# Optimization experiments

Hardware: AMD Instinct MI355X
Metric: run time of the kernel (lower is better)

The kernel has to match this reference:

```python
import jax, jax.numpy as jnp
import numpy as np

B, S, D = 4, 2048, 1024
H = 16
DH = D // H


def setup_inputs() -> dict:
    key = jax.random.key(0)
    ks = jax.random.split(key, 9)
    s = 0.02
    return {
        "x": jax.random.normal(ks[0], (B, S, D), dtype=jnp.float32),
        "Wq": jax.random.normal(ks[1], (D, D), dtype=jnp.float32) * s,
        "bq": jax.random.normal(ks[2], (D,), dtype=jnp.float32) * s,
        "Wk": jax.random.normal(ks[3], (D, D), dtype=jnp.float32) * s,
        "bk": jax.random.normal(ks[4], (D,), dtype=jnp.float32) * s,
        "Wv": jax.random.normal(ks[5], (D, D), dtype=jnp.float32) * s,
        "bv": jax.random.normal(ks[6], (D,), dtype=jnp.float32) * s,
        "Wo": jax.random.normal(ks[7], (D, D), dtype=jnp.float32) * s,
        "bo": jax.random.normal(ks[8], (D,), dtype=jnp.float32) * s,
    }


def _split_heads(t):
    # [B,S,D] -> [B,H,S,DH]
    b, s, d = t.shape
    return t.reshape(b, s, H, DH).transpose(0, 2, 1, 3)


def reference(x, Wq, bq, Wk, bk, Wv, bv, Wo, bo):
    q = _split_heads(x @ Wq.T + bq)
    k = _split_heads(x @ Wk.T + bk)
    v = _split_heads(x @ Wv.T + bv)
    scale = 1.0 / np.sqrt(DH).astype(np.float32)
    scores = jnp.einsum("bhqd,bhkd->bhqk", q, k) * scale  # [B,H,S,S]
    s = scores.shape[-2]
    causal = jnp.tril(jnp.ones((s, s), dtype=bool))
    scores = jnp.where(causal[None, None], scores, -jnp.inf)
    probs = jax.nn.softmax(scores, axis=-1)
    out = jnp.einsum("bhqk,bhkd->bhqd", probs, v)  # [B,H,S,DH]
    out = out.transpose(0, 2, 1, 3).reshape(x.shape[0], s, D)
    return out @ Wo.T + bo
```

## Files before the change

### kernel.cpp

```cpp
#include <hip/hip_runtime.h>
#include <hip/hip_bf16.h>
#include <cstdint>
#include <cstddef>


typedef unsigned short u16;
typedef __bf16 bf16x8 __attribute__((ext_vector_type(8)));
typedef float  f32x4  __attribute__((ext_vector_type(4)));

__device__ __forceinline__ u16 f2bf(float f) {
  unsigned u = __float_as_uint(f);
  unsigned r = u + 0x7fffu + ((u >> 16) & 1u);
  return (u16)(r >> 16);
}

__device__ __forceinline__ void llds16(const u16* g, u16* l) {
  __builtin_amdgcn_global_load_lds(
      (const __attribute__((address_space(1))) void*)g,
      (__attribute__((address_space(3))) void*)l, 16, 0, 0);
}

__global__ void cast_bf16_kernel(const float* __restrict__ in, u16* __restrict__ out, int n4) {
  int i = blockIdx.x * blockDim.x + threadIdx.x;
  if (i >= n4) return;
  float4 f = ((const float4*)in)[i];
  ushort4 u;
  u.x = f2bf(f.x); u.y = f2bf(f.y); u.z = f2bf(f.z); u.w = f2bf(f.w);
  ((ushort4*)out)[i] = u;
}

__global__ void cast4_kernel(const float* __restrict__ a, const float* __restrict__ b,
                             const float* __restrict__ c, const float* __restrict__ d,
                             u16* __restrict__ oa, u16* __restrict__ ob,
                             u16* __restrict__ oc, u16* __restrict__ od, int n4) {
  const int w = blockIdx.y;
  const float* src = (w == 0) ? a : (w == 1) ? b : (w == 2) ? c : d;
  u16* dst = (w == 0) ? oa : (w == 1) ? ob : (w == 2) ? oc : od;
  int i = blockIdx.x * blockDim.x + threadIdx.x;
  if (i >= n4) return;
  float4 f = ((const float4*)src)[i];
  ushort4 u;
  u.x = f2bf(f.x); u.y = f2bf(f.y); u.z = f2bf(f.z); u.w = f2bf(f.w);
  ((ushort4*)dst)[i] = u;
}

__global__ __launch_bounds__(512) void gemm_qkv_256(
    const u16* __restrict__ A, const u16* __restrict__ Bw,
    const float* __restrict__ b0, const float* __restrict__ b1, const float* __restrict__ b2,
    u16* __restrict__ qkv_out)
{
  __shared__ u16 lds[57344];

  const int tid = threadIdx.x;
  const int lane = tid & 63;
  const int wave = tid >> 6;

  const int bid = (int)blockIdx.x;
  const int xcd = bid & 7;
  const int idx = bid >> 3;
  const int mt = (xcd << 2) | (idx & 3);
  const int nt = idx >> 2;
  const int m0 = mt << 8;
  const int n0 = nt * 192;

  const int warp_m = wave >> 2;
  const int warp_n = wave & 3;
  const int wm = warp_m << 7;
  const int wn = warp_n * 48;
  const int fr = lane & 15;
  const int g  = lane >> 4;

  const int srow = tid >> 3;
  const int schk = ((tid & 7) ^ (srow & 7)) << 3;
  const u16* pA = A  + (size_t)(m0 + srow) * 1024 + schk;
  const u16* pB = Bw + (size_t)(n0 + srow) * 1024 + schk;

  const int rsw0 = ((g    ) ^ (fr & 7)) << 3;
  const int rsw1 = ((g ^ 4) ^ (fr & 7)) << 3;

  const u16* Ab0 = lds + (size_t)(wm + fr) * 64;
  const u16* Bb0 = lds + 16384 + (size_t)(wn + fr) * 64;
  const u16* Ab1 = Ab0 + 28672;
  const u16* Bb1 = Bb0 + 28672;

  f32x4 acc[8][3];
  const f32x4 zero = {0.f, 0.f, 0.f, 0.f};
#pragma unroll
  for (int i = 0; i < 8; i++)
#pragma unroll
    for (int j = 0; j < 3; j++) acc[i][j] = zero;

  bf16x8 a_[8][2];
  bf16x8 b_[3][2];

  auto stageA = [&](int kt, int buf, int half) {
    const u16* src = pA + (size_t)half * 131072 + (kt << 6);
    u16* dst = lds + buf * 28672 + half * 8192 + tid * 8;
    llds16(src, dst);
    llds16(src + 65536, dst + 4096);
  };
  auto stageB0 = [&](int kt, int buf) {
    const u16* src = pB + (kt << 6);
    u16* dst = lds + buf * 28672 + 16384 + tid * 8;
    llds16(src, dst);
    llds16(src + 65536, dst + 4096);
  };
  auto stageB1 = [&](int kt, int buf) {
    const u16* src = pB + 131072 + (kt << 6);
    u16* dst = lds + buf * 28672 + 24576 + tid * 8;
    llds16(src, dst);
  };
  auto loadA4 = [&](const u16* Ab, int ib) {
#pragma unroll
    for (int ii = 0; ii < 4; ii++) {
      const u16* r = Ab + (ib + ii) * 1024;
      a_[ib + ii][0] = *(const bf16x8*)(r + rsw0);
      a_[ib + ii][1] = *(const bf16x8*)(r + rsw1);
    }
  };
  auto loadB = [&](const u16* Bb, int j0, int nj) {
#pragma unroll
    for (int jj = 0; jj < 3; jj++) {
      if (jj < nj) {
        const u16* r = Bb + (j0 + jj) * 1024;
        b_[j0 + jj][0] = *(const bf16x8*)(r + rsw0);
        b_[j0 + jj][1] = *(const bf16x8*)(r + rsw1);
      }
    }
  };
  auto mfmaJ01 = [&](int ib) {
    __builtin_amdgcn_s_setprio(1);
#pragma unroll
    for (int jj = 0; jj < 2; jj++)
#pragma unroll
      for (int ii = 0; ii < 4; ii++) {
        acc[ib+ii][jj] = __builtin_amdgcn_mfma_f32_16x16x32_bf16(
            a_[ib+ii][0], b_[jj][0], acc[ib+ii][jj], 0, 0, 0);
        acc[ib+ii][jj] = __builtin_amdgcn_mfma_f32_16x16x32_bf16(
            a_[ib+ii][1], b_[jj][1], acc[ib+ii][jj], 0, 0, 0);
      }
    __builtin_amdgcn_s_setprio(0);
  };
  auto mfmaJ2 = [&]() {
    __builtin_amdgcn_s_setprio(1);
#pragma unroll
    for (int ii = 0; ii < 8; ii++) {
      acc[ii][2] = __builtin_amdgcn_mfma_f32_16x16x32_bf16(
          a_[ii][0], b_[2][0], acc[ii][2], 0, 0, 0);
      acc[ii][2] = __builtin_amdgcn_mfma_f32_16x16x32_bf16(
          a_[ii][1], b_[2][1], acc[ii][2], 0, 0, 0);
    }
    __builtin_amdgcn_s_setprio(0);
  };

  stageA(0, 0, 0);
  stageA(0, 0, 1);
  stageB0(0, 0);
  stageB1(0, 0);
  stageA(1, 1, 0);
  asm volatile("s_waitcnt vmcnt(2)" ::: "memory");
  __builtin_amdgcn_s_barrier();

  const int NTI = 8;
  for (int t = 0; t < NTI; ++t) {
    const bool st = (t < NTI - 1);
    const int ka = 2 * t + 1;
    const int kb = 2 * t + 2;
    const int kc = 2 * t + 3;

    loadA4(Ab0, 0); loadB(Bb0, 0, 2);
    stageA(ka, 1, 1);
    __builtin_amdgcn_s_barrier();
    mfmaJ01(0);
    __builtin_amdgcn_s_barrier();
    loadA4(Ab0, 4);
    stageB0(ka, 1);
    __builtin_amdgcn_s_barrier();
    mfmaJ01(4);
    __builtin_amdgcn_s_barrier();
    loadB(Bb0, 2, 1);
    stageB1(ka, 1);
    if (st) stageA(kb, 0, 0);
    __builtin_amdgcn_s_barrier();
    mfmaJ2();
    if (st) { asm volatile("s_waitcnt vmcnt(2)" ::: "memory"); }
    else    { asm volatile("s_waitcnt vmcnt(0)" ::: "memory"); }
    __builtin_amdgcn_s_barrier();

    loadA4(Ab1, 0); loadB(Bb1, 0, 2);
    if (st) stageA(kb, 0, 1);
    __builtin_amdgcn_s_barrier();
    mfmaJ01(0);
    __builtin_amdgcn_s_barrier();
    loadA4(Ab1, 4);
    if (st) stageB0(kb, 0);
    __builtin_amdgcn_s_barrier();
    mfmaJ01(4);
    __builtin_amdgcn_s_barrier();
    loadB(Bb1, 2, 1);
    if (st) { stageB1(kb, 0); stageA(kc, 1, 0); }
    __builtin_amdgcn_s_barrier();
    mfmaJ2();
    if (st) { asm volatile("s_waitcnt vmcnt(2)" ::: "memory"); }
    __builtin_amdgcn_s_barrier();
  }

  __syncthreads();
  const int bI  = m0 >> 11;
  const int s0m = m0 & 2047;
#pragma unroll
  for (int j = 0; j < 3; j++) {
    const int ncol = n0 + wn + j * 16 + fr;
    const int which = ncol >> 10;
    const float bb = ((which == 0) ? b0 : (which == 1) ? b1 : b2)[ncol & 1023];
    const float post = (which == 0) ? 0.18033688011f : 1.0f;
    const int cl = wn + j * 16 + fr;
#pragma unroll
    for (int i = 0; i < 8; i++) {
#pragma unroll
      for (int r = 0; r < 4; r++) {
        const int row = wm + i * 16 + g * 4 + r;
        lds[row * 200 + cl] = f2bf((acc[i][j][r] + bb) * post);
      }
    }
  }
  __syncthreads();
  const int part = tid & 7;
#pragma unroll
  for (int p = 0; p < 12; p++) {
    const int hc = p >> 2;
    const int ml = ((p & 3) << 6) + (tid >> 3);
    const int ncol0 = n0 + hc * 64;
    const int which = ncol0 >> 10;
    const int h = (ncol0 >> 6) & 15;
    const bf16x8 v = *(const bf16x8*)(lds + ml * 200 + hc * 64 + part * 8);
    *(bf16x8*)(qkv_out + (size_t)which * 8388608 +
               ((size_t)(bI * 16 + h) * 2048 + s0m + ml) * 64 + part * 8) = v;
  }
}

__global__ __launch_bounds__(512) void gemm_o_256(
    const u16* __restrict__ A, const u16* __restrict__ Bw,
    const float* __restrict__ bo, float* __restrict__ out)
{
  __shared__ u16 lds[49152];

  const int tid = threadIdx.x;
  const int lane = tid & 63;
  const int wave = tid >> 6;

  const int bid = (int)blockIdx.x;
  const int xcd = bid & 7;
  const int idx = bid >> 3;
  const int mt = (xcd << 2) | (idx & 3);
  const int nt = idx >> 2;
  const int m0 = mt << 8;
  const int n0 = nt << 7;

  const int warp_m = wave >> 2;
  const int warp_n = wave & 3;
  const int wm = warp_m << 7;
  const int wn = warp_n << 5;
  const int fr = lane & 15;
  const int g  = lane >> 4;

  const int srow = tid >> 3;
  const int schk = ((tid & 7) ^ (srow & 7)) << 3;
  const u16* pA = A  + (size_t)(m0 + srow) * 1024 + schk;
  const u16* pB = Bw + (size_t)(n0 + srow) * 1024 + schk;

  const int rsw0 = ((g    ) ^ (fr & 7)) << 3;
  const int rsw1 = ((g ^ 4) ^ (fr & 7)) << 3;

  const u16* Ab0 = lds + (size_t)(wm + fr) * 64;
  const u16* Bb0 = lds + 16384 + (size_t)(wn + fr) * 64;
  const u16* Ab1 = Ab0 + 24576;
  const u16* Bb1 = Bb0 + 24576;

  f32x4 acc[8][2];
  const f32x4 zero = {0.f, 0.f, 0.f, 0.f};
#pragma unroll
  for (int i = 0; i < 8; i++)
#pragma unroll
    for (int j = 0; j < 2; j++) acc[i][j] = zero;

  bf16x8 a_[8][2];
  bf16x8 b_[2][2];

  auto stageA = [&](int kt, int buf, int half) {
    const u16* src = pA + (size_t)half * 131072 + (kt << 6);
    u16* dst = lds + buf * 24576 + half * 8192 + tid * 8;
    llds16(src, dst);
    llds16(src + 65536, dst + 4096);
  };
  auto stageB = [&](int kt, int buf) {
    const u16* src = pB + (kt << 6);
    u16* dst = lds + buf * 24576 + 16384 + tid * 8;
    llds16(src, dst);
    llds16(src + 65536, dst + 4096);
  };
  auto loadA4 = [&](const u16* Ab, int ib) {
#pragma unroll
    for (int ii = 0; ii < 4; ii++) {
      const u16* r = Ab + (ib + ii) * 1024;
      a_[ib + ii][0] = *(const bf16x8*)(r + rsw0);
      a_[ib + ii][1] = *(const bf16x8*)(r + rsw1);
    }
  };
  auto loadB2 = [&](const u16* Bb) {
#pragma unroll
    for (int jj = 0; jj < 2; jj++) {
      const u16* r = Bb + jj * 1024;
      b_[jj][0] = *(const bf16x8*)(r + rsw0);
      b_[jj][1] = *(const bf16x8*)(r + rsw1);
    }
  };
  auto mfma16 = [&](int ib) {
    __builtin_amdgcn_s_setprio(1);
#pragma unroll
    for (int jj = 0; jj < 2; jj++)
#pragma unroll
      for (int ii = 0; ii < 4; ii++) {
        acc[ib+ii][jj] = __builtin_amdgcn_mfma_f32_16x16x32_bf16(
            a_[ib+ii][0], b_[jj][0], acc[ib+ii][jj], 0, 0, 0);
        acc[ib+ii][jj] = __builtin_amdgcn_mfma_f32_16x16x32_bf16(
            a_[ib+ii][1], b_[jj][1], acc[ib+ii][jj], 0, 0, 0);
      }
    __builtin_amdgcn_s_setprio(0);
  };
  auto mfma8 = [&](int ib, int jj) {
    __builtin_amdgcn_s_setprio(1);
#pragma unroll
    for (int ii = 0; ii < 4; ii++) {
      acc[ib+ii][jj] = __builtin_amdgcn_mfma_f32_16x16x32_bf16(
          a_[ib+ii][0], b_[jj][0], acc[ib+ii][jj], 0, 0, 0);
      acc[ib+ii][jj] = __builtin_amdgcn_mfma_f32_16x16x32_bf16(
          a_[ib+ii][1], b_[jj][1], acc[ib+ii][jj], 0, 0, 0);
    }
    __builtin_amdgcn_s_setprio(0);
  };

  stageA(0, 0, 0);
  stageA(0, 0, 1);
  stageB(0, 0);
  stageA(1, 1, 0);
  asm volatile("s_waitcnt vmcnt(2)" ::: "memory");
  __builtin_amdgcn_s_barrier();

  const int NTI = 8;
  for (int t = 0; t < NTI; ++t) {
    const bool st = (t < NTI - 1);
    const int ka = 2 * t + 1;
    const int kb = 2 * t + 2;
    const int kc = 2 * t + 3;

    loadA4(Ab0, 0); loadB2(Bb0);
    stageA(ka, 1, 1);
    __builtin_amdgcn_s_barrier();
    mfma16(0);
    __builtin_amdgcn_s_barrier();
    loadA4(Ab0, 4);
    stageB(ka, 1);
    __builtin_amdgcn_s_barrier();
    mfma8(4, 0);
    __builtin_amdgcn_s_barrier();
    if (st) stageA(kb, 0, 0);
    __builtin_amdgcn_s_barrier();
    mfma8(4, 1);
    if (st) { asm volatile("s_waitcnt vmcnt(2)" ::: "memory"); }
    else    { asm volatile("s_waitcnt vmcnt(0)" ::: "memory"); }
    __builtin_amdgcn_s_barrier();

    loadA4(Ab1, 0); loadB2(Bb1);
    if (st) stageA(kb, 0, 1);
    __builtin_amdgcn_s_barrier();
    mfma16(0);
    __builtin_amdgcn_s_barrier();
    loadA4(Ab1, 4);
    if (st) stageB(kb, 0);
    __builtin_amdgcn_s_barrier();
    mfma8(4, 0);
    __builtin_amdgcn_s_barrier();
    if (st) stageA(kc, 1, 0);
    __builtin_amdgcn_s_barrier();
    mfma8(4, 1);
    if (st) { asm volatile("s_waitcnt vmcnt(2)" ::: "memory"); }
    __builtin_amdgcn_s_barrier();
  }

#pragma unroll
  for (int j = 0; j < 2; j++) {
    const int n = n0 + wn + j * 16 + fr;
    const float bb = bo[n];
#pragma unroll
    for (int i = 0; i < 8; i++) {
#pragma unroll
      for (int r = 0; r < 4; r++) {
        const int m = m0 + wm + i * 16 + g * 4 + r;
        out[(size_t)m * 1024 + n] = acc[i][j][r] + bb;
      }
    }
  }
}

__global__ __launch_bounds__(256) void transpose_v(const u16* __restrict__ V, u16* __restrict__ VT) {
  __shared__ u16 t_s[64 * 72];
  const int tid = threadIdx.x;
  const int st = blockIdx.x << 6;
  const int bh = blockIdx.y;
  const u16* src = V + ((size_t)bh * 2048 + st) * 64;
#pragma unroll
  for (int p = 0; p < 2; p++) {
    int i = p * 256 + tid;
    int row = i >> 3, ch = i & 7;
    bf16x8 v = *(const bf16x8*)(src + row * 64 + ch * 8);
    *(bf16x8*)(t_s + row * 72 + ch * 8) = v;
  }
  __syncthreads();
  u16* dst = VT + (size_t)bh * 131072 + st;
#pragma unroll
  for (int p = 0; p < 2; p++) {
    int i = p * 256 + tid;
    int dh = i >> 3, ch = i & 7;
    union { u16 s[8]; bf16x8 v; } u;
#pragma unroll
    for (int e = 0; e < 8; e++) u.s[e] = t_s[(ch * 8 + e) * 72 + dh];
    *(bf16x8*)(dst + (size_t)dh * 2048 + ch * 8) = u.v;
  }
}

__global__ __launch_bounds__(256, 3) void attn_fa(
    const u16* __restrict__ Qb, const u16* __restrict__ Kb,
    const u16* __restrict__ VT, u16* __restrict__ Ob)
{
  __shared__ u16 k_s[2 * 4096];
  __shared__ u16 v_s[2 * 4096];
  __shared__ u16 p_s[128 * 72];
  __shared__ float l_s[128];

  const int tid = threadIdx.x;
  const int lane = tid & 63;
  const int wave = tid >> 6;
  const int bid = (int)blockIdx.x;
  const int qt = 15 - (bid >> 6);
  const int bh = (((bid >> 3) & 7) << 3) | (bid & 7);
  const size_t head = (size_t)bh << 17;
  const int fr = lane & 15;
  const int g = lane >> 4;
  const int k8 = g << 3;
  const int q0 = qt << 7;
  const int wrow = wave << 5;

  bf16x8 aq[2][2];
#pragma unroll
  for (int f = 0; f < 2; f++) {
    const u16* qp = Qb + head + (size_t)(q0 + wrow + (f << 4) + fr) * 64;
    aq[f][0] = *(const bf16x8*)(qp + k8);
    aq[f][1] = *(const bf16x8*)(qp + 32 + k8);
  }

  const int r0 = tid >> 3, c0 = tid & 7;
  const int r1 = 32 + r0;
  const int koff0 = r0 * 64 + (((c0 ^ r0) & 7) << 3);
  const int koff1 = r1 * 64 + (((c0 ^ r1) & 7) << 3);
  const int voff0 = r0 * 2048 + (((c0 ^ r0) & 7) << 3);
  const int voff1 = r1 * 2048 + (((c0 ^ r1) & 7) << 3);
  int kaddr[4][2], vaddr[2][4];
#pragma unroll
  for (int j = 0; j < 4; j++) {
    const int kn = (j << 4) + fr;
    kaddr[j][0] = kn * 64 + (((g ^ kn) & 7) << 3);
    kaddr[j][1] = kn * 64 + ((((g + 4) ^ kn) & 7) << 3);
#pragma unroll
    for (int s2 = 0; s2 < 2; s2++)
      vaddr[s2][j] = kn * 64 + ((((s2 << 2) + g) ^ (kn & 7)) << 3);
  }
  u16* const prow0 = p_s + (wrow + fr) * 72;
  u16* const prow1 = p_s + (wrow + 16 + fr) * 72;
  const u16* Kbase = Kb + head;
  const u16* Vbase = VT + head;

  auto issueK = [&](int jt2, int buf) {
    const u16* Kt = Kbase + ((size_t)jt2 << 12);
    llds16(Kt + koff0, k_s + (buf << 12) + tid * 8);
    llds16(Kt + koff1, k_s + (buf << 12) + 2048 + tid * 8);
  };
  auto issueV = [&](int jt2, int buf) {
    const u16* Vt = Vbase + (jt2 << 6);
    llds16(Vt + voff0, v_s + (buf << 12) + tid * 8);
    llds16(Vt + voff1, v_s + (buf << 12) + 2048 + tid * 8);
  };

  f32x4 o_acc[2][4];
  const f32x4 zero = {0.f, 0.f, 0.f, 0.f};
#pragma unroll
  for (int f = 0; f < 2; f++)
#pragma unroll
    for (int j = 0; j < 4; j++) o_acc[f][j] = zero;
  float l_run[2] = {0.f, 0.f};

  const int jmax = 2 * qt + 1;
  const int jt_diag = 2 * qt + (wave >> 1);

  auto do_pv = [&](const u16* vs) {
#pragma unroll
    for (int s2 = 0; s2 < 2; s2++) {
      const bf16x8 ap0 = *(const bf16x8*)(prow0 + (s2 << 5) + k8);
      const bf16x8 ap1 = *(const bf16x8*)(prow1 + (s2 << 5) + k8);
#pragma unroll
      for (int j = 0; j < 4; j++) {
        const bf16x8 bv = *(const bf16x8*)(vs + vaddr[s2][j]);
        o_acc[0][j] = __builtin_amdgcn_mfma_f32_16x16x32_bf16(ap0, bv, o_acc[0][j], 0, 0, 0);
        o_acc[1][j] = __builtin_amdgcn_mfma_f32_16x16x32_bf16(ap1, bv, o_acc[1][j], 0, 0, 0);
      }
    }
  };

  auto do_s = [&](const u16* ks, bool dodiag, int jt) {
    f32x4 s_acc[2][4];
#pragma unroll
    for (int f = 0; f < 2; f++)
#pragma unroll
      for (int j = 0; j < 4; j++) s_acc[f][j] = zero;
#pragma unroll
    for (int j = 0; j < 4; j++) {
      const bf16x8 ka0 = *(const bf16x8*)(ks + kaddr[j][0]);
      const bf16x8 ka1 = *(const bf16x8*)(ks + kaddr[j][1]);
      s_acc[0][j] = __builtin_amdgcn_mfma_f32_16x16x32_bf16(ka0, aq[0][0], s_acc[0][j], 0, 0, 0);
      s_acc[0][j] = __builtin_amdgcn_mfma_f32_16x16x32_bf16(ka1, aq[0][1], s_acc[0][j], 0, 0, 0);
      s_acc[1][j] = __builtin_amdgcn_mfma_f32_16x16x32_bf16(ka0, aq[1][0], s_acc[1][j], 0, 0, 0);
      s_acc[1][j] = __builtin_amdgcn_mfma_f32_16x16x32_bf16(ka1, aq[1][1], s_acc[1][j], 0, 0, 0);
    }
#pragma unroll
    for (int f = 0; f < 2; f++) {
      const int qa = q0 + wrow + (f << 4) + fr;
      u16* prow = (f == 0) ? prow0 : prow1;
      if (dodiag) {
#pragma unroll
        for (int j = 0; j < 4; j++) {
          const int kb = (jt << 6) + (j << 4) + (g << 2);
          float p0 = (kb + 0 > qa) ? 0.f : __builtin_amdgcn_exp2f(s_acc[f][j][0]);
          float p1 = (kb + 1 > qa) ? 0.f : __builtin_amdgcn_exp2f(s_acc[f][j][1]);
          float p2 = (kb + 2 > qa) ? 0.f : __builtin_amdgcn_exp2f(s_acc[f][j][2]);
          float p3 = (kb + 3 > qa) ? 0.f : __builtin_amdgcn_exp2f(s_acc[f][j][3]);
          l_run[f] += (p0 + p1) + (p2 + p3);
          union { __hip_bfloat162 h; unsigned u; } ca, cb;
          ca.h = __float22bfloat162_rn(make_float2(p0, p1));
          cb.h = __float22bfloat162_rn(make_float2(p2, p3));
          *(uint2*)(prow + (j << 4) + (g << 2)) = make_uint2(ca.u, cb.u);
        }
      } else {
#pragma unroll
        for (int j = 0; j < 4; j++) {
          float p0 = __builtin_amdgcn_exp2f(s_acc[f][j][0]);
          float p1 = __builtin_amdgcn_exp2f(s_acc[f][j][1]);
          float p2 = __builtin_amdgcn_exp2f(s_acc[f][j][2]);
          float p3 = __builtin_amdgcn_exp2f(s_acc[f][j][3]);
          l_run[f] += (p0 + p1) + (p2 + p3);
          union { __hip_bfloat162 h; unsigned u; } ca, cb;
          ca.h = __float22bfloat162_rn(make_float2(p0, p1));
          cb.h = __float22bfloat162_rn(make_float2(p2, p3));
          *(uint2*)(prow + (j << 4) + (g << 2)) = make_uint2(ca.u, cb.u);
        }
      }
    }
  };

  issueK(0, 0);

  for (int jt = 0; jt <= jmax; jt++) {
    const int kb = jt & 1;
    __syncthreads();
    if (jt < jmax) issueK(jt + 1, kb ^ 1);
    issueV(jt, kb);
    if (jt > 0 && jt - 1 <= jt_diag) do_pv(v_s + ((kb ^ 1) << 12));
    if (jt <= jt_diag) do_s(k_s + (kb << 12), jt == jt_diag, jt);
  }
  __syncthreads();
  if (jt_diag == jmax) do_pv(v_s + ((jmax & 1) << 12));

#pragma unroll
  for (int f = 0; f < 2; f++) {
    float l = l_run[f];
    l += __shfl_xor(l, 16);
    l += __shfl_xor(l, 32);
    if (g == 0) l_s[wrow + (f << 4) + fr] = l;
  }
  const int b = bh >> 4, h = bh & 15;
#pragma unroll
  for (int f = 0; f < 2; f++) {
#pragma unroll
    for (int r = 0; r < 4; r++) {
      const int qloc = wrow + (f << 4) + (g << 2) + r;
      const float inv = 1.f / l_s[qloc];
      const int q_abs = q0 + qloc;
#pragma unroll
      for (int j = 0; j < 4; j++)
        Ob[((size_t)b * 2048 + q_abs) * 1024 + (h << 6) + (j << 4) + fr] =
            f2bf(o_acc[f][j][r] * inv);
    }
  }
}

extern "C" void kernel_launch(void* const* d_in, const int* in_sizes, int n_in,
                              void* d_out, int out_size, void* d_ws, size_t ws_size,
                              hipStream_t stream) {
  const float* x  = (const float*)d_in[0];
  const float* Wq = (const float*)d_in[1];
  const float* bq = (const float*)d_in[2];
  const float* Wk = (const float*)d_in[3];
  const float* bk = (const float*)d_in[4];
  const float* Wv = (const float*)d_in[5];
  const float* bv = (const float*)d_in[6];
  const float* Wo = (const float*)d_in[7];
  const float* bo = (const float*)d_in[8];
  float* out = (float*)d_out;

  char* ws = (char*)d_ws;
  u16* xb    = (u16*)(ws);
  u16* vT    = (u16*)(ws);
  u16* wqkv  = (u16*)(ws + 16777216);
  u16* wo    = (u16*)(ws + 23068672);
  u16* qkv   = (u16*)(ws + 25165824);
  u16* attnb = (u16*)(ws + 75497472);

  cast_bf16_kernel<<<8192, 256, 0, stream>>>(x, xb, 2097152);
  cast4_kernel<<<dim3(1024, 4), 256, 0, stream>>>(
      Wq, Wk, Wv, Wo, wqkv, wqkv + 1048576, wqkv + 2097152, wo, 262144);

  gemm_qkv_256<<<dim3(512), 512, 0, stream>>>(xb, wqkv, bq, bk, bv, qkv);

  transpose_v<<<dim3(32, 64), 256, 0, stream>>>(qkv + 16777216, vT);

  attn_fa<<<dim3(1024), 256, 0, stream>>>(qkv, qkv + 8388608, vT, attnb);

  gemm_o_256<<<dim3(256), 512, 0, stream>>>(attnb, wo, bo, out);
}
```

Baseline: 242.0 us.

## Merge cast kernels and reorder QKV GEMM into quadrant MFMA phases

Replaces the separate activation and weight cast kernels with a single launch covering x and all four weights, removing one kernel launch. The QKV GEMM inner loop is restructured into quadrant phases (4 A-rows by 1-2 B-columns) so only four A fragments are live at once, reducing register pressure at the cost of extra barriers and a different load/stage interleaving. The attention output buffer is aliased onto the V region of qkv, which assumes V is no longer needed once transposed into vT.

```diff
diff --git a/kernel.cpp b/kernel.cpp
--- a/kernel.cpp
+++ b/kernel.cpp
@@ -20,28 +20,30 @@
       (__attribute__((address_space(3))) void*)l, 16, 0, 0);
 }
 
-__global__ void cast_bf16_kernel(const float* __restrict__ in, u16* __restrict__ out, int n4) {
-  int i = blockIdx.x * blockDim.x + threadIdx.x;
-  if (i >= n4) return;
-  float4 f = ((const float4*)in)[i];
-  ushort4 u;
-  u.x = f2bf(f.x); u.y = f2bf(f.y); u.z = f2bf(f.z); u.w = f2bf(f.w);
-  ((ushort4*)out)[i] = u;
-}
-
-__global__ void cast4_kernel(const float* __restrict__ a, const float* __restrict__ b,
-                             const float* __restrict__ c, const float* __restrict__ d,
-                             u16* __restrict__ oa, u16* __restrict__ ob,
-                             u16* __restrict__ oc, u16* __restrict__ od, int n4) {
-  const int w = blockIdx.y;
-  const float* src = (w == 0) ? a : (w == 1) ? b : (w == 2) ? c : d;
-  u16* dst = (w == 0) ? oa : (w == 1) ? ob : (w == 2) ? oc : od;
-  int i = blockIdx.x * blockDim.x + threadIdx.x;
-  if (i >= n4) return;
-  float4 f = ((const float4*)src)[i];
-  ushort4 u;
-  u.x = f2bf(f.x); u.y = f2bf(f.y); u.z = f2bf(f.z); u.w = f2bf(f.w);
-  ((ushort4*)dst)[i] = u;
+__global__ void cast_all_kernel(const float* __restrict__ x,
+                                const float* __restrict__ Wq, const float* __restrict__ Wk,
+                                const float* __restrict__ Wv, const float* __restrict__ Wo,
+                                u16* __restrict__ xb, u16* __restrict__ wqkv,
+                                u16* __restrict__ wo) {
+  const int bid = (int)blockIdx.x;
+  const int tid = threadIdx.x;
+  if (bid < 8192) {
+    const int i = (bid << 8) + tid;
+    float4 f = ((const float4*)x)[i];
+    ushort4 u;
+    u.x = f2bf(f.x); u.y = f2bf(f.y); u.z = f2bf(f.z); u.w = f2bf(f.w);
+    ((ushort4*)xb)[i] = u;
+  } else {
+    const int j = ((bid - 8192) << 8) + tid;
+    const int w = j >> 18;
+    const int idx = j & 262143;
+    const float* src = (w == 0) ? Wq : (w == 1) ? Wk : (w == 2) ? Wv : Wo;
+    u16* dst = (w == 3) ? wo : (wqkv + (w << 20));
+    float4 f = ((const float4*)src)[idx];
+    ushort4 u;
+    u.x = f2bf(f.x); u.y = f2bf(f.y); u.z = f2bf(f.z); u.w = f2bf(f.w);
+    ((ushort4*)dst)[idx] = u;
+  }
 }
 
 __global__ __launch_bounds__(512) void gemm_qkv_256(
@@ -90,7 +92,7 @@
 #pragma unroll
     for (int j = 0; j < 3; j++) acc[i][j] = zero;
 
-  bf16x8 a_[8][2];
+  bf16x8 a_[4][2];
   bf16x8 b_[3][2];
 
   auto stageA = [&](int kt, int buf, int half) {
@@ -114,8 +116,8 @@
 #pragma unroll
     for (int ii = 0; ii < 4; ii++) {
       const u16* r = Ab + (ib + ii) * 1024;
-      a_[ib + ii][0] = *(const bf16x8*)(r + rsw0);
-      a_[ib + ii][1] = *(const bf16x8*)(r + rsw1);
+      a_[ii][0] = *(const bf16x8*)(r + rsw0);
+      a_[ii][1] = *(const bf16x8*)(r + rsw1);
     }
   };
   auto loadB = [&](const u16* Bb, int j0, int nj) {
@@ -128,27 +130,19 @@
       }
     }
   };
-  auto mfmaJ01 = [&](int ib) {
+  auto mfmaQ = [&](int ib, int j0, int nj) {
     __builtin_amdgcn_s_setprio(1);
 #pragma unroll
-    for (int jj = 0; jj < 2; jj++)
-#pragma unroll
-      for (int ii = 0; ii < 4; ii++) {
-        acc[ib+ii][jj] = __builtin_amdgcn_mfma_f32_16x16x32_bf16(
-            a_[ib+ii][0], b_[jj][0], acc[ib+ii][jj], 0, 0, 0);
-        acc[ib+ii][jj] = __builtin_amdgcn_mfma_f32_16x16x32_bf16(
-            a_[ib+ii][1], b_[jj][1], acc[ib+ii][jj], 0, 0, 0);
+    for (int jj = 0; jj < 3; jj++) {
+      if (jj < nj) {
+#pragma unroll
+        for (int ii = 0; ii < 4; ii++) {
+          acc[ib+ii][j0+jj] = __builtin_amdgcn_mfma_f32_16x16x32_bf16(
+              a_[ii][0], b_[j0+jj][0], acc[ib+ii][j0+jj], 0, 0, 0);
+          acc[ib+ii][j0+jj] = __builtin_amdgcn_mfma_f32_16x16x32_bf16(
+              a_[ii][1], b_[j0+jj][1], acc[ib+ii][j0+jj], 0, 0, 0);
+        }
       }
-    __builtin_amdgcn_s_setprio(0);
-  };
-  auto mfmaJ2 = [&]() {
-    __builtin_amdgcn_s_setprio(1);
-#pragma unroll
-    for (int ii = 0; ii < 8; ii++) {
-      acc[ii][2] = __builtin_amdgcn_mfma_f32_16x16x32_bf16(
-          a_[ii][0], b_[2][0], acc[ii][2], 0, 0, 0);
-      acc[ii][2] = __builtin_amdgcn_mfma_f32_16x16x32_bf16(
-          a_[ii][1], b_[2][1], acc[ii][2], 0, 0, 0);
     }
     __builtin_amdgcn_s_setprio(0);
   };
@@ -171,18 +165,21 @@
     loadA4(Ab0, 0); loadB(Bb0, 0, 2);
     stageA(ka, 1, 1);
     __builtin_amdgcn_s_barrier();
-    mfmaJ01(0);
+    mfmaQ(0, 0, 2);
+    __builtin_amdgcn_s_barrier();
+    loadB(Bb0, 2, 1);
+    stageB0(ka, 1);
+    __builtin_amdgcn_s_barrier();
+    mfmaQ(0, 2, 1);
     __builtin_amdgcn_s_barrier();
     loadA4(Ab0, 4);
-    stageB0(ka, 1);
-    __builtin_amdgcn_s_barrier();
-    mfmaJ01(4);
-    __builtin_amdgcn_s_barrier();
-    loadB(Bb0, 2, 1);
     stageB1(ka, 1);
+    __builtin_amdgcn_s_barrier();
+    mfmaQ(4, 2, 1);
+    __builtin_amdgcn_s_barrier();
     if (st) stageA(kb, 0, 0);
     __builtin_amdgcn_s_barrier();
-    mfmaJ2();
+    mfmaQ(4, 0, 2);
     if (st) { asm volatile("s_waitcnt vmcnt(2)" ::: "memory"); }
     else    { asm volatile("s_waitcnt vmcnt(0)" ::: "memory"); }
     __builtin_amdgcn_s_barrier();
@@ -190,17 +187,21 @@
     loadA4(Ab1, 0); loadB(Bb1, 0, 2);
     if (st) stageA(kb, 0, 1);
     __builtin_amdgcn_s_barrier();
-    mfmaJ01(0);
+    mfmaQ(0, 0, 2);
+    __builtin_amdgcn_s_barrier();
+    loadB(Bb1, 2, 1);
+    if (st) stageB0(kb, 0);
+    __builtin_amdgcn_s_barrier();
+    mfmaQ(0, 2, 1);
     __builtin_amdgcn_s_barrier();
     loadA4(Ab1, 4);
-    if (st) stageB0(kb, 0);
-    __builtin_amdgcn_s_barrier();
-    mfmaJ01(4);
-    __builtin_amdgcn_s_barrier();
-    loadB(Bb1, 2, 1);
-    if (st) { stageB1(kb, 0); stageA(kc, 1, 0); }
-    __builtin_amdgcn_s_barrier();
-    mfmaJ2();
+    if (st) stageB1(kb, 0);
+    __builtin_amdgcn_s_barrier();
+    mfmaQ(4, 2, 1);
+    __builtin_amdgcn_s_barrier();
+    if (st) stageA(kc, 1, 0);
+    __builtin_amdgcn_s_barrier();
+    mfmaQ(4, 0, 2);
     if (st) { asm volatile("s_waitcnt vmcnt(2)" ::: "memory"); }
     __builtin_amdgcn_s_barrier();
   }
@@ -622,11 +623,9 @@
   u16* wqkv  = (u16*)(ws + 16777216);
   u16* wo    = (u16*)(ws + 23068672);
   u16* qkv   = (u16*)(ws + 25165824);
-  u16* attnb = (u16*)(ws + 75497472);
-
-  cast_bf16_kernel<<<8192, 256, 0, stream>>>(x, xb, 2097152);
-  cast4_kernel<<<dim3(1024, 4), 256, 0, stream>>>(
-      Wq, Wk, Wv, Wo, wqkv, wqkv + 1048576, wqkv + 2097152, wo, 262144);
+  u16* attnb = qkv + 16777216;
+
+  cast_all_kernel<<<12288, 256, 0, stream>>>(x, Wq, Wk, Wv, Wo, xb, wqkv, wo);
 
   gemm_qkv_256<<<dim3(512), 512, 0, stream>>>(xb, wqkv, bq, bk, bv, qkv);
 
```

Result: no change. 238.7 us (-1.4%).
